# Performance work log

Measured on AMD Instinct MI355X. Metric: run time of the kernel, lower is better.

## Reference

```python
import jax, jax.numpy as jnp
import numpy as np

B, N, H, EH = 4, 512, 128, 128


def _init_linear(key, fan_in, fan_out, scale=0.02):
    W = jax.random.normal(key, (fan_in, fan_out), dtype=jnp.float32) * scale
    b = jnp.zeros((fan_out,), dtype=jnp.float32)
    return W, b


def setup_inputs() -> dict:
    key = jax.random.key(0)
    ks = jax.random.split(key, 9)
    h = jax.random.normal(ks[0], (B, N, H), dtype=jnp.float32)
    x = jax.random.normal(ks[1], (B, N, 3), dtype=jnp.float32)
    We1, be1 = _init_linear(ks[2], 2 * H + 1, EH)
    We2, be2 = _init_linear(ks[3], EH, H)
    Wc1, bc1 = _init_linear(ks[4], H, EH)
    Wc2, bc2 = _init_linear(ks[5], EH, 1)
    Wc2 = Wc2 * 0.1  # coord_mlp[-1].weight.mul_(0.1)
    Wn1, bn1 = _init_linear(ks[6], 2 * H, EH)
    Wn2, bn2 = _init_linear(ks[7], EH, H)
    return {
        "h": h, "x": x,
        "We1": We1, "be1": be1, "We2": We2, "be2": be2,
        "Wc1": Wc1, "bc1": bc1, "Wc2": Wc2, "bc2": bc2,
        "Wn1": Wn1, "bn1": bn1, "Wn2": Wn2, "bn2": bn2,
        "radius": 2,
    }


def reference(h, x, We1, be1, We2, be2, Wc1, bc1, Wc2, bc2, Wn1, bn1, Wn2, bn2, radius):
    silu = jax.nn.silu
    Hd = h.shape[-1]
    # pairwise geometry
    dx = x[:, :, None, :] - x[:, None, :, :]            # [B,N,N,3]
    d2 = jnp.sum(dx * dx, axis=-1, keepdims=True)       # [B,N,N,1]
    n = h.shape[1]
    eye = jnp.eye(n, dtype=bool)[None]                  # [1,N,N]
    mask = (d2[..., 0] < float(radius) ** 2) & ~eye     # [B,N,N]
    mask_f = mask[..., None].astype(h.dtype)            # [B,N,N,1]
    # edge MLP: split concat([h_i,h_j,d2]) @ We1 into three small matmuls
    pre = (jnp.einsum('bnh,he->bne', h, We1[:Hd])[:, :, None, :]
           + jnp.einsum('bnh,he->bne', h, We1[Hd:2 * Hd])[:, None, :, :]
           + d2 * We1[2 * Hd] + be1)                    # [B,N,N,EH]
    m_ij = silu(silu(pre) @ We2 + be2) * mask_f          # [B,N,N,H]
    agg = m_ij.sum(axis=2)                               # [B,N,H]
    # coord update
    gate = silu(m_ij @ Wc1 + bc1) @ Wc2 + bc2            # [B,N,N,1]
    coord_delta = jnp.sum(dx * gate * mask_f, axis=2)    # [B,N,3]
    n_neighbors = jnp.clip(mask.sum(axis=-1, keepdims=True), 1, None).astype(dx.dtype)
    x_new = x + coord_delta / n_neighbors
    # node update
    h_cat = jnp.concatenate([h, agg], axis=-1)           # [B,N,2H]
    h_new = h + (silu(h_cat @ Wn1 + bn1) @ Wn2 + bn2)
    return h_new, x_new
```

## Files before the change

kernel.cpp:

```cpp
#include <hip/hip_runtime.h>

#define BB 4
#define NN 512
#define HH 128
#define EHH 128
#define JB 64

typedef short short8 __attribute__((ext_vector_type(8)));
typedef float f32x4 __attribute__((ext_vector_type(4)));

__device__ __forceinline__ float fsilu(float x){
    float e = __expf(-x);
    return x * __builtin_amdgcn_rcpf(1.0f + e);
}

__device__ __forceinline__ unsigned int cvt_pk_bf16(float lo, float hi){
    unsigned int r;
    asm("v_cvt_pk_bf16_f32 %0, %1, %2" : "=v"(r) : "v"(lo), "v"(hi));
    return r;
}

__device__ __forceinline__ unsigned short f2bf(float f){
    return (unsigned short)(cvt_pk_bf16(f, 0.f) & 0xffffu);
}

__device__ __forceinline__ unsigned int cvt_pk_fp8(float lo, float hi){
    unsigned int r;
    asm("v_cvt_pk_fp8_f32 %0, %1, %2" : "=v"(r) : "v"(lo), "v"(hi));
    return r;
}

__global__ __launch_bounds__(256) void k_prep(
    const float* __restrict__ h,
    const float* __restrict__ We1, const float* __restrict__ be1,
    const float* __restrict__ We2, const float* __restrict__ Wc1,
    float* __restrict__ hi_e, unsigned short* __restrict__ hj_eb,
    unsigned short* __restrict__ We2T, unsigned char* __restrict__ Wc1F8)
{
    const int tid = threadIdx.x;
    if (blockIdx.x < BB*NN/8) {
        __shared__ float hrows[8][HH];
        const int row0 = blockIdx.x * 8;
        #pragma unroll
        for (int t = tid; t < 8*HH; t += 256)
            hrows[t >> 7][t & 127] = h[row0*HH + t];
        __syncthreads();
        const int col  = tid & 127;
        const int half = tid >> 7;
        float acc[8] = {0.f,0.f,0.f,0.f,0.f,0.f,0.f,0.f};
        #pragma unroll 4
        for (int k = 0; k < HH; ++k){
            float w = We1[(half*HH + k)*EHH + col];
            #pragma unroll
            for (int r = 0; r < 8; ++r) acc[r] += hrows[r][k] * w;
        }
        if (half == 0){
            const float bb = be1[col];
            #pragma unroll
            for (int r = 0; r < 8; ++r)
                hi_e[(row0 + r)*EHH + col] = acc[r] + bb;
        } else {
            #pragma unroll
            for (int r = 0; r < 8; ++r)
                hj_eb[(row0 + r)*EHH + col] = f2bf(acc[r]);
        }
    } else {
        const int bid = blockIdx.x - BB*NN/8;
        for (int t = bid*256 + tid; t < 128*128; t += 16*256){
            int o = t >> 7, kk = t & 127;
            We2T[t] = f2bf(We2[kk*HH + o]);
        }
        for (int idx = bid*256 + tid; idx < 8192; idx += 16*256){
            int o = idx >> 6, kp = idx & 63;
            int k = 2*kp;
            unsigned int pk = cvt_pk_fp8(Wc1[k*EHH + o] * 16.f,
                                         Wc1[(k+1)*EHH + o] * 16.f);
            *(unsigned short*)&Wc1F8[o*EHH + k] = (unsigned short)(pk & 0xffffu);
        }
    }
}

__global__ __launch_bounds__(256, 2) void k_edge(
    const float* __restrict__ x,
    const float* __restrict__ hi_e,
    const unsigned short* __restrict__ hj_eb,
    const unsigned short* __restrict__ We2T,
    const unsigned char* __restrict__ Wc1F8,
    const float* __restrict__ We1,
    const float* __restrict__ be2,
    const float* __restrict__ bc1,
    const float* __restrict__ wc2,
    const float* __restrict__ bc2p,
    const int* __restrict__ radius,
    float* __restrict__ aggb, float* __restrict__ xout)
{
    __shared__ unsigned short A1[JB][136];
    __shared__ unsigned char  mA8[JB][136];
    __shared__ float dxs[2][JB][4];
    __shared__ float his[HH], w3s[HH];
    __shared__ float aggp[2][HH];
    __shared__ float cred[4][3];
    __shared__ unsigned short jseg[4][128];
    __shared__ unsigned short jlist[NN];
    __shared__ int cnts[4];

    const int tid  = threadIdx.x;
    const int lane = tid & 63;
    const int wave = tid >> 6;
    const int l15  = lane & 15;
    const int g    = lane >> 4;
    const int wm   = wave >> 1, wn = wave & 1;

    const int b = blockIdx.x >> 9;
    const int i = blockIdx.x & (NN-1);
    const int base = b*NN;

    if (tid < HH){
        his[tid] = hi_e[(base + i)*EHH + tid];
        w3s[tid] = We1[2*HH*EHH + tid];
    }
    const float xi0 = x[(base+i)*3+0];
    const float xi1 = x[(base+i)*3+1];
    const float xi2 = x[(base+i)*3+2];
    const int   rad = radius[0];
    const float r2  = (float)(rad*rad);
    const float bc2v = bc2p[0];

    float be2r[4], bc1r[4], wc2r[4];
    #pragma unroll
    for (int nt = 0; nt < 4; ++nt){
        const int col = wn*64 + nt*16 + l15;
        be2r[nt] = be2[col];
        bc1r[nt] = bc1[col];
        wc2r[nt] = wc2[col];
    }

    short8 bW1[4][4];
    long   bW2[4][4];
    #pragma unroll
    for (int nt = 0; nt < 4; ++nt){
        const int col = wn*64 + nt*16 + l15;
        #pragma unroll
        for (int ks = 0; ks < 4; ++ks){
            bW1[nt][ks] = *(const short8*)&We2T[col*EHH + ks*32 + g*8];
            bW2[nt][ks] = *(const long*)&Wc1F8[col*EHH + ks*32 + g*8];
        }
    }

    int wcnt = 0;
    #pragma unroll
    for (int t = 0; t < 2; ++t){
        const int j = wave*128 + t*64 + lane;
        float xj0 = x[(base+j)*3+0];
        float xj1 = x[(base+j)*3+1];
        float xj2 = x[(base+j)*3+2];
        float d0 = xi0-xj0, d1 = xi1-xj1, d2c = xi2-xj2;
        float d2v = d0*d0 + d1*d1 + d2c*d2c;
        bool pass = (d2v < r2) && (j != i);
        unsigned long long bal = __ballot(pass);
        int pos = __popcll(bal & ((1ull << lane) - 1ull));
        if (pass) jseg[wave][wcnt + pos] = (unsigned short)j;
        wcnt += __popcll(bal);
    }
    if (lane == 0) cnts[wave] = wcnt;
    __syncthreads();
    const int c0n = cnts[0], c1n = cnts[1], c2n = cnts[2], c3n = cnts[3];
    const int total = c0n + c1n + c2n + c3n;
    const int off = (wave > 0 ? c0n : 0) + (wave > 1 ? c1n : 0) + (wave > 2 ? c2n : 0);
    for (int k2 = lane; k2 < wcnt; k2 += 64)
        jlist[off + k2] = jseg[wave][k2];
    __syncthreads();

    const int nch = (total + JB - 1) / JB;

    float agg[4] = {0.f, 0.f, 0.f, 0.f};
    float cx = 0.f, cy = 0.f, cz = 0.f;

    short8 hjn[4];
    float xjn0 = 0.f, xjn1 = 0.f, xjn2 = 0.f, mfn = 0.f;
    if (nch > 0){
        const int idx = lane;
        const int vld = idx < total;
        const int jn = vld ? jlist[idx] : jlist[total-1];
        mfn = vld ? 1.f : 0.f;
        #pragma unroll
        for (int k = 0; k < 4; ++k)
            hjn[k] = *(const short8*)&hj_eb[(base + jn)*EHH + wave*32 + k*8];
        xjn0 = x[(base+jn)*3+0];
        xjn1 = x[(base+jn)*3+1];
        xjn2 = x[(base+jn)*3+2];
    }

    #pragma unroll 1
    for (int c = 0; c < nch; ++c){
        const int buf = c & 1;
        const int r = lane;

        float d0 = xi0 - xjn0;
        float d1 = xi1 - xjn1;
        float d2c = xi2 - xjn2;
        float d2v = d0*d0 + d1*d1 + d2c*d2c;
        float mf = mfn;
        if (wave == 0){
            dxs[buf][r][0] = d0; dxs[buf][r][1] = d1;
            dxs[buf][r][2] = d2c; dxs[buf][r][3] = mf;
            float t = mf * bc2v;
            cx += d0*t; cy += d1*t; cz += d2c*t;
        }
        const int sw = ((r>>3)&1)<<3;
        #pragma unroll
        for (int k = 0; k < 4; ++k){
            const int c0 = wave*32 + k*8;
            short8 hj8 = hjn[k];
            f32x4 hiA = *(const f32x4*)&his[c0];
            f32x4 hiB = *(const f32x4*)&his[c0+4];
            f32x4 w3A = *(const f32x4*)&w3s[c0];
            f32x4 w3B = *(const f32x4*)&w3s[c0+4];
            float p[8];
            #pragma unroll
            for (int e = 0; e < 4; ++e){
                float hv0 = __uint_as_float(((unsigned int)(unsigned short)hj8[e]) << 16);
                float hv1 = __uint_as_float(((unsigned int)(unsigned short)hj8[e+4]) << 16);
                p[e]   = fsilu(hiA[e] + hv0 + d2v*w3A[e]);
                p[e+4] = fsilu(hiB[e] + hv1 + d2v*w3B[e]);
            }
            short8 outv;
            ((unsigned int*)&outv)[0] = cvt_pk_bf16(p[0], p[1]);
            ((unsigned int*)&outv)[1] = cvt_pk_bf16(p[2], p[3]);
            ((unsigned int*)&outv)[2] = cvt_pk_bf16(p[4], p[5]);
            ((unsigned int*)&outv)[3] = cvt_pk_bf16(p[6], p[7]);
            *(short8*)&A1[r][c0 ^ sw] = outv;
        }
        if (c + 1 < nch){
            const int idx = (c+1)*JB + lane;
            const int vld = idx < total;
            const int jn = vld ? jlist[idx] : jlist[total-1];
            mfn = vld ? 1.f : 0.f;
            #pragma unroll
            for (int k = 0; k < 4; ++k)
                hjn[k] = *(const short8*)&hj_eb[(base + jn)*EHH + wave*32 + k*8];
            xjn0 = x[(base+jn)*3+0];
            xjn1 = x[(base+jn)*3+1];
            xjn2 = x[(base+jn)*3+2];
        }
        __syncthreads();

        f32x4 acc[2][4];
        #pragma unroll
        for (int mt = 0; mt < 2; ++mt)
            #pragma unroll
            for (int nt = 0; nt < 4; ++nt) acc[mt][nt] = (f32x4){0.f,0.f,0.f,0.f};

        const int swr = ((l15>>3)&1)<<3;
        #pragma unroll
        for (int ks = 0; ks < 4; ++ks){
            short8 afr[2];
            #pragma unroll
            for (int mt = 0; mt < 2; ++mt){
                const int row = wm*32 + mt*16 + l15;
                afr[mt] = *(const short8*)&A1[row][(ks*32 + g*8) ^ swr];
            }
            #pragma unroll
            for (int nt = 0; nt < 4; ++nt)
                #pragma unroll
                for (int mt = 0; mt < 2; ++mt)
                    acc[mt][nt] = __builtin_amdgcn_mfma_f32_16x16x32_bf16(
                        afr[mt], bW1[nt][ks], acc[mt][nt], 0, 0, 0);
        }

        #pragma unroll
        for (int mt = 0; mt < 2; ++mt){
            float mfr[4];
            #pragma unroll
            for (int rg = 0; rg < 4; ++rg)
                mfr[rg] = dxs[buf][wm*32 + mt*16 + g*4 + rg][3];
            #pragma unroll
            for (int nt = 0; nt < 4; ++nt){
                const int col = wn*64 + nt*16 + l15;
                f32x4 v = acc[mt][nt];
                #pragma unroll
                for (int rg = 0; rg < 4; ++rg){
                    const int row = wm*32 + mt*16 + g*4 + rg;
                    float m = fsilu(v[rg] + be2r[nt]) * mfr[rg];
                    agg[nt] += m;
                    mA8[row][col] = (unsigned char)(cvt_pk_fp8(m * 8.f, 0.f) & 0xffu);
                }
            }
        }
        __syncthreads();

        f32x4 acc2[2][4];
        #pragma unroll
        for (int mt = 0; mt < 2; ++mt)
            #pragma unroll
            for (int nt = 0; nt < 4; ++nt) acc2[mt][nt] = (f32x4){0.f,0.f,0.f,0.f};

        #pragma unroll
        for (int ks = 0; ks < 4; ++ks){
            long a8[2];
            #pragma unroll
            for (int mt = 0; mt < 2; ++mt){
                const int row = wm*32 + mt*16 + l15;
                a8[mt] = *(const long*)&mA8[row][ks*32 + g*8];
            }
            #pragma unroll
            for (int nt = 0; nt < 4; ++nt)
                #pragma unroll
                for (int mt = 0; mt < 2; ++mt)
                    acc2[mt][nt] = __builtin_amdgcn_mfma_f32_16x16x32_fp8_fp8(
                        a8[mt], bW2[nt][ks], acc2[mt][nt], 0, 0, 0);
        }

        float gp[2][4];
        #pragma unroll
        for (int mt = 0; mt < 2; ++mt)
            #pragma unroll
            for (int rg = 0; rg < 4; ++rg) gp[mt][rg] = 0.f;
        #pragma unroll
        for (int mt = 0; mt < 2; ++mt)
            #pragma unroll
            for (int nt = 0; nt < 4; ++nt){
                f32x4 v = acc2[mt][nt];
                #pragma unroll
                for (int rg = 0; rg < 4; ++rg)
                    gp[mt][rg] += fsilu(v[rg]*(1.f/128.f) + bc1r[nt]) * wc2r[nt];
            }
        #pragma unroll
        for (int mt = 0; mt < 2; ++mt)
            #pragma unroll
            for (int rg = 0; rg < 4; ++rg){
                const int row = wm*32 + mt*16 + g*4 + rg;
                f32x4 dv = *(const f32x4*)&dxs[buf][row][0];
                float gv = gp[mt][rg] * dv[3];
                cx += dv[0]*gv; cy += dv[1]*gv; cz += dv[2]*gv;
            }
    }

    #pragma unroll
    for (int nt = 0; nt < 4; ++nt){
        float t = agg[nt];
        t += __shfl_xor(t, 16); t += __shfl_xor(t, 32);
        agg[nt] = t;
    }
    if (lane < 16){
        #pragma unroll
        for (int nt = 0; nt < 4; ++nt)
            aggp[wm][wn*64 + nt*16 + l15] = agg[nt];
    }

    #pragma unroll
    for (int m = 1; m <= 32; m <<= 1){
        cx += __shfl_xor(cx, m);
        cy += __shfl_xor(cy, m);
        cz += __shfl_xor(cz, m);
    }
    if (lane == 0){
        cred[wave][0] = cx; cred[wave][1] = cy; cred[wave][2] = cz;
    }
    __syncthreads();
    if (tid < HH) aggb[(base + i)*HH + tid] = aggp[0][tid] + aggp[1][tid];
    if (tid == 0){
        float sx = cred[0][0] + cred[1][0] + cred[2][0] + cred[3][0];
        float sy = cred[0][1] + cred[1][1] + cred[2][1] + cred[3][1];
        float sz = cred[0][2] + cred[1][2] + cred[2][2] + cred[3][2];
        float inv = 1.0f / (float)(total > 0 ? total : 1);
        xout[(base+i)*3 + 0] = xi0 + sx*inv;
        xout[(base+i)*3 + 1] = xi1 + sy*inv;
        xout[(base+i)*3 + 2] = xi2 + sz*inv;
    }
}

__global__ __launch_bounds__(128) void k_node(
    const float* __restrict__ h, const float* __restrict__ aggb,
    const float* __restrict__ Wn1, const float* __restrict__ bn1,
    const float* __restrict__ Wn2, const float* __restrict__ bn2,
    float* __restrict__ hout)
{
    __shared__ float hcat[8][260];
    __shared__ float t1[8][132];
    const int tid = threadIdx.x;
    const int row0 = blockIdx.x * 8;
    #pragma unroll
    for (int r = 0; r < 8; ++r){
        hcat[r][tid]      = h[(row0 + r)*HH + tid];
        hcat[r][HH + tid] = aggb[(row0 + r)*HH + tid];
    }
    __syncthreads();
    float acc[8] = {0.f,0.f,0.f,0.f,0.f,0.f,0.f,0.f};
    #pragma unroll 4
    for (int k = 0; k < 2*HH; ++k){
        float w = Wn1[k*EHH + tid];
        #pragma unroll
        for (int r = 0; r < 8; ++r) acc[r] += hcat[r][k] * w;
    }
    const float bn1v = bn1[tid];
    #pragma unroll
    for (int r = 0; r < 8; ++r) t1[r][tid] = fsilu(acc[r] + bn1v);
    __syncthreads();
    float acc2[8] = {0.f,0.f,0.f,0.f,0.f,0.f,0.f,0.f};
    #pragma unroll 4
    for (int e = 0; e < EHH; ++e){
        float w = Wn2[e*HH + tid];
        #pragma unroll
        for (int r = 0; r < 8; ++r) acc2[r] += t1[r][e] * w;
    }
    const float bn2v = bn2[tid];
    #pragma unroll
    for (int r = 0; r < 8; ++r)
        hout[(row0 + r)*HH + tid] = hcat[r][tid] + acc2[r] + bn2v;
}

extern "C" void kernel_launch(void* const* d_in, const int* in_sizes, int n_in,
                              void* d_out, int out_size, void* d_ws, size_t ws_size,
                              hipStream_t stream) {
    const float* h   = (const float*)d_in[0];
    const float* x   = (const float*)d_in[1];
    const float* We1 = (const float*)d_in[2];
    const float* be1 = (const float*)d_in[3];
    const float* We2 = (const float*)d_in[4];
    const float* be2 = (const float*)d_in[5];
    const float* Wc1 = (const float*)d_in[6];
    const float* bc1 = (const float*)d_in[7];
    const float* Wc2 = (const float*)d_in[8];
    const float* bc2 = (const float*)d_in[9];
    const float* Wn1 = (const float*)d_in[10];
    const float* bn1 = (const float*)d_in[11];
    const float* Wn2 = (const float*)d_in[12];
    const float* bn2 = (const float*)d_in[13];
    const int* radius = (const int*)d_in[14];

    float* out_h = (float*)d_out;
    float* out_x = out_h + BB*NN*HH;

    char* ws = (char*)d_ws;
    float*          hi_e  = (float*)ws;
    unsigned short* hj_eb = (unsigned short*)(ws + (1u<<20));
    unsigned short* We2T  = (unsigned short*)(ws + (1u<<20) + (512u<<10));
    unsigned char*  Wc1F8 = (unsigned char*)(ws + (1u<<20) + (544u<<10));
    float*          aggb  = (float*)(ws + (1u<<20) + (560u<<10));

    k_prep<<<BB*NN/8 + 16, 256, 0, stream>>>(h, We1, be1, We2, Wc1,
                                             hi_e, hj_eb, We2T, Wc1F8);
    k_edge<<<BB*NN, 256, 0, stream>>>(x, hi_e, hj_eb, We2T, Wc1F8,
                                      We1, be2, bc1, Wc2, bc2, radius,
                                      aggb, out_x);
    k_node<<<BB*NN/8, 128, 0, stream>>>(h, aggb, Wn1, bn1, Wn2, bn2, out_h);
}
```

Before: 236.8 us.

## Process one node per wave with 16-neighbor chunks and shared LDS weights

The edge kernel now gives each wave its own node i, so one 256-thread block handles four nodes. Each wave walks its own neighbor list in chunks of 16 and computes all 128 output columns itself. The bf16 and fp8 weight matrices are staged once per block into shared memory instead of being held in per-wave registers. Intermediate A fragments stay in registers and the per-chunk block barriers disappear, so waves no longer synchronise with each other. The cost is many more LDS reads of the B weights per MFMA, smaller MFMA tiles per chunk, and per-wave load imbalance when neighbor counts differ.

```diff
diff --git a/kernel.cpp b/kernel.cpp
--- a/kernel.cpp
+++ b/kernel.cpp
@@ -4,10 +4,11 @@
 #define NN 512
 #define HH 128
 #define EHH 128
-#define JB 64
+#define JC 16
 
 typedef short short8 __attribute__((ext_vector_type(8)));
 typedef float f32x4 __attribute__((ext_vector_type(4)));
+typedef int   int4v __attribute__((ext_vector_type(4)));
 
 __device__ __forceinline__ float fsilu(float x){
     float e = __expf(-x);
@@ -94,30 +95,45 @@
     const int* __restrict__ radius,
     float* __restrict__ aggb, float* __restrict__ xout)
 {
-    __shared__ unsigned short A1[JB][136];
-    __shared__ unsigned char  mA8[JB][136];
-    __shared__ float dxs[2][JB][4];
-    __shared__ float his[HH], w3s[HH];
-    __shared__ float aggp[2][HH];
-    __shared__ float cred[4][3];
-    __shared__ unsigned short jseg[4][128];
-    __shared__ unsigned short jlist[NN];
-    __shared__ int cnts[4];
+    __shared__ unsigned short We2T_s[128][136];
+    __shared__ unsigned char  Wc1F8_s[128][144];
+    __shared__ unsigned short jlist[4][NN];
+    __shared__ unsigned char  mA8[4][JC][136];
 
     const int tid  = threadIdx.x;
     const int lane = tid & 63;
     const int wave = tid >> 6;
     const int l15  = lane & 15;
     const int g    = lane >> 4;
-    const int wm   = wave >> 1, wn = wave & 1;
-
-    const int b = blockIdx.x >> 9;
-    const int i = blockIdx.x & (NN-1);
-    const int base = b*NN;
-
-    if (tid < HH){
-        his[tid] = hi_e[(base + i)*EHH + tid];
-        w3s[tid] = We1[2*HH*EHH + tid];
+
+    const int b    = blockIdx.x >> 7;
+    const int i    = (blockIdx.x & 127) * 4 + wave;
+    const int base = b * NN;
+
+    for (int t = tid; t < 128*16; t += 256){
+        int row = t >> 4, seg = t & 15;
+        *(short8*)&We2T_s[row][seg*8] = *(const short8*)&We2T[row*EHH + seg*8];
+    }
+    for (int t = tid; t < 128*8; t += 256){
+        int row = t >> 3, seg = t & 7;
+        *(int4v*)&Wc1F8_s[row][seg*16] = *(const int4v*)&Wc1F8[row*EHH + seg*16];
+    }
+
+    f32x4 hiA[4], hiB[4], w3A[4], w3B[4];
+    #pragma unroll
+    for (int ks = 0; ks < 4; ++ks){
+        hiA[ks] = *(const f32x4*)&hi_e[(base+i)*EHH + ks*32 + g*8];
+        hiB[ks] = *(const f32x4*)&hi_e[(base+i)*EHH + ks*32 + g*8 + 4];
+        w3A[ks] = *(const f32x4*)&We1[2*HH*EHH + ks*32 + g*8];
+        w3B[ks] = *(const f32x4*)&We1[2*HH*EHH + ks*32 + g*8 + 4];
+    }
+    float be2r[8], bc1r[8], wc2r[8];
+    #pragma unroll
+    for (int nt = 0; nt < 8; ++nt){
+        const int col = nt*16 + l15;
+        be2r[nt] = be2[col];
+        bc1r[nt] = bc1[col];
+        wc2r[nt] = wc2[col];
     }
     const float xi0 = x[(base+i)*3+0];
     const float xi1 = x[(base+i)*3+1];
@@ -126,31 +142,10 @@
     const float r2  = (float)(rad*rad);
     const float bc2v = bc2p[0];
 
-    float be2r[4], bc1r[4], wc2r[4];
-    #pragma unroll
-    for (int nt = 0; nt < 4; ++nt){
-        const int col = wn*64 + nt*16 + l15;
-        be2r[nt] = be2[col];
-        bc1r[nt] = bc1[col];
-        wc2r[nt] = wc2[col];
-    }
-
-    short8 bW1[4][4];
-    long   bW2[4][4];
-    #pragma unroll
-    for (int nt = 0; nt < 4; ++nt){
-        const int col = wn*64 + nt*16 + l15;
-        #pragma unroll
-        for (int ks = 0; ks < 4; ++ks){
-            bW1[nt][ks] = *(const short8*)&We2T[col*EHH + ks*32 + g*8];
-            bW2[nt][ks] = *(const long*)&Wc1F8[col*EHH + ks*32 + g*8];
-        }
-    }
-
-    int wcnt = 0;
-    #pragma unroll
-    for (int t = 0; t < 2; ++t){
-        const int j = wave*128 + t*64 + lane;
+    int cnt = 0;
+    #pragma unroll 1
+    for (int t = 0; t < NN/64; ++t){
+        const int j = t*64 + lane;
         float xj0 = x[(base+j)*3+0];
         float xj1 = x[(base+j)*3+1];
         float xj2 = x[(base+j)*3+2];
@@ -159,214 +154,157 @@
         bool pass = (d2v < r2) && (j != i);
         unsigned long long bal = __ballot(pass);
         int pos = __popcll(bal & ((1ull << lane) - 1ull));
-        if (pass) jseg[wave][wcnt + pos] = (unsigned short)j;
-        wcnt += __popcll(bal);
-    }
-    if (lane == 0) cnts[wave] = wcnt;
+        if (pass) jlist[wave][cnt + pos] = (unsigned short)j;
+        cnt += __popcll(bal);
+    }
+
     __syncthreads();
-    const int c0n = cnts[0], c1n = cnts[1], c2n = cnts[2], c3n = cnts[3];
-    const int total = c0n + c1n + c2n + c3n;
-    const int off = (wave > 0 ? c0n : 0) + (wave > 1 ? c1n : 0) + (wave > 2 ? c2n : 0);
-    for (int k2 = lane; k2 < wcnt; k2 += 64)
-        jlist[off + k2] = jseg[wave][k2];
-    __syncthreads();
-
-    const int nch = (total + JB - 1) / JB;
-
-    float agg[4] = {0.f, 0.f, 0.f, 0.f};
+
+    const int nch = (cnt + JC - 1) / JC;
+
+    float agg[8] = {0.f,0.f,0.f,0.f,0.f,0.f,0.f,0.f};
     float cx = 0.f, cy = 0.f, cz = 0.f;
 
-    short8 hjn[4];
-    float xjn0 = 0.f, xjn1 = 0.f, xjn2 = 0.f, mfn = 0.f;
+    short8 hjp[4];
+    float xjp0 = 0.f, xjp1 = 0.f, xjp2 = 0.f;
     if (nch > 0){
-        const int idx = lane;
-        const int vld = idx < total;
-        const int jn = vld ? jlist[idx] : jlist[total-1];
-        mfn = vld ? 1.f : 0.f;
-        #pragma unroll
-        for (int k = 0; k < 4; ++k)
-            hjn[k] = *(const short8*)&hj_eb[(base + jn)*EHH + wave*32 + k*8];
-        xjn0 = x[(base+jn)*3+0];
-        xjn1 = x[(base+jn)*3+1];
-        xjn2 = x[(base+jn)*3+2];
+        int idx = l15 < cnt ? l15 : cnt-1;
+        int jn = jlist[wave][idx];
+        #pragma unroll
+        for (int ks = 0; ks < 4; ++ks)
+            hjp[ks] = *(const short8*)&hj_eb[(base+jn)*EHH + ks*32 + g*8];
+        xjp0 = x[(base+jn)*3+0];
+        xjp1 = x[(base+jn)*3+1];
+        xjp2 = x[(base+jn)*3+2];
     }
 
     #pragma unroll 1
     for (int c = 0; c < nch; ++c){
-        const int buf = c & 1;
-        const int r = lane;
-
-        float d0 = xi0 - xjn0;
-        float d1 = xi1 - xjn1;
-        float d2c = xi2 - xjn2;
+        float d0 = xi0 - xjp0;
+        float d1 = xi1 - xjp1;
+        float d2c = xi2 - xjp2;
         float d2v = d0*d0 + d1*d1 + d2c*d2c;
-        float mf = mfn;
-        if (wave == 0){
-            dxs[buf][r][0] = d0; dxs[buf][r][1] = d1;
-            dxs[buf][r][2] = d2c; dxs[buf][r][3] = mf;
-            float t = mf * bc2v;
-            cx += d0*t; cy += d1*t; cz += d2c*t;
-        }
-        const int sw = ((r>>3)&1)<<3;
-        #pragma unroll
-        for (int k = 0; k < 4; ++k){
-            const int c0 = wave*32 + k*8;
-            short8 hj8 = hjn[k];
-            f32x4 hiA = *(const f32x4*)&his[c0];
-            f32x4 hiB = *(const f32x4*)&his[c0+4];
-            f32x4 w3A = *(const f32x4*)&w3s[c0];
-            f32x4 w3B = *(const f32x4*)&w3s[c0+4];
+        short8 a1[4];
+        #pragma unroll
+        for (int ks = 0; ks < 4; ++ks){
+            short8 hj8 = hjp[ks];
             float p[8];
             #pragma unroll
             for (int e = 0; e < 4; ++e){
                 float hv0 = __uint_as_float(((unsigned int)(unsigned short)hj8[e]) << 16);
                 float hv1 = __uint_as_float(((unsigned int)(unsigned short)hj8[e+4]) << 16);
-                p[e]   = fsilu(hiA[e] + hv0 + d2v*w3A[e]);
-                p[e+4] = fsilu(hiB[e] + hv1 + d2v*w3B[e]);
+                p[e]   = fsilu(hiA[ks][e] + hv0 + d2v*w3A[ks][e]);
+                p[e+4] = fsilu(hiB[ks][e] + hv1 + d2v*w3B[ks][e]);
             }
             short8 outv;
             ((unsigned int*)&outv)[0] = cvt_pk_bf16(p[0], p[1]);
             ((unsigned int*)&outv)[1] = cvt_pk_bf16(p[2], p[3]);
             ((unsigned int*)&outv)[2] = cvt_pk_bf16(p[4], p[5]);
             ((unsigned int*)&outv)[3] = cvt_pk_bf16(p[6], p[7]);
-            *(short8*)&A1[r][c0 ^ sw] = outv;
+            a1[ks] = outv;
         }
         if (c + 1 < nch){
-            const int idx = (c+1)*JB + lane;
-            const int vld = idx < total;
-            const int jn = vld ? jlist[idx] : jlist[total-1];
-            mfn = vld ? 1.f : 0.f;
-            #pragma unroll
-            for (int k = 0; k < 4; ++k)
-                hjn[k] = *(const short8*)&hj_eb[(base + jn)*EHH + wave*32 + k*8];
-            xjn0 = x[(base+jn)*3+0];
-            xjn1 = x[(base+jn)*3+1];
-            xjn2 = x[(base+jn)*3+2];
-        }
-        __syncthreads();
-
-        f32x4 acc[2][4];
-        #pragma unroll
-        for (int mt = 0; mt < 2; ++mt)
-            #pragma unroll
-            for (int nt = 0; nt < 4; ++nt) acc[mt][nt] = (f32x4){0.f,0.f,0.f,0.f};
-
-        const int swr = ((l15>>3)&1)<<3;
+            int idx = (c+1)*JC + l15;
+            idx = idx < cnt ? idx : cnt-1;
+            int jn = jlist[wave][idx];
+            #pragma unroll
+            for (int ks = 0; ks < 4; ++ks)
+                hjp[ks] = *(const short8*)&hj_eb[(base+jn)*EHH + ks*32 + g*8];
+            xjp0 = x[(base+jn)*3+0];
+            xjp1 = x[(base+jn)*3+1];
+            xjp2 = x[(base+jn)*3+2];
+        }
+
+        f32x4 acc1[8];
+        #pragma unroll
+        for (int nt = 0; nt < 8; ++nt) acc1[nt] = (f32x4){0.f,0.f,0.f,0.f};
         #pragma unroll
         for (int ks = 0; ks < 4; ++ks){
-            short8 afr[2];
-            #pragma unroll
-            for (int mt = 0; mt < 2; ++mt){
-                const int row = wm*32 + mt*16 + l15;
-                afr[mt] = *(const short8*)&A1[row][(ks*32 + g*8) ^ swr];
-            }
-            #pragma unroll
-            for (int nt = 0; nt < 4; ++nt)
-                #pragma unroll
-                for (int mt = 0; mt < 2; ++mt)
-                    acc[mt][nt] = __builtin_amdgcn_mfma_f32_16x16x32_bf16(
-                        afr[mt], bW1[nt][ks], acc[mt][nt], 0, 0, 0);
-        }
-
-        #pragma unroll
-        for (int mt = 0; mt < 2; ++mt){
-            float mfr[4];
+            #pragma unroll
+            for (int nt = 0; nt < 8; ++nt){
+                short8 bf = *(const short8*)&We2T_s[nt*16 + l15][ks*32 + g*8];
+                acc1[nt] = __builtin_amdgcn_mfma_f32_16x16x32_bf16(
+                    a1[ks], bf, acc1[nt], 0, 0, 0);
+            }
+        }
+
+        float mfr[4];
+        #pragma unroll
+        for (int rg = 0; rg < 4; ++rg)
+            mfr[rg] = (c*JC + 4*g + rg < cnt) ? 1.f : 0.f;
+        #pragma unroll
+        for (int nt = 0; nt < 8; ++nt){
+            f32x4 v = acc1[nt];
+            #pragma unroll
+            for (int rg = 0; rg < 4; ++rg){
+                float m = fsilu(v[rg] + be2r[nt]) * mfr[rg];
+                agg[nt] += m;
+                mA8[wave][4*g + rg][nt*16 + l15] =
+                    (unsigned char)(cvt_pk_fp8(m * 8.f, 0.f) & 0xffu);
+            }
+        }
+
+        long a8[4];
+        #pragma unroll
+        for (int ks = 0; ks < 4; ++ks)
+            a8[ks] = *(const long*)&mA8[wave][l15][ks*32 + g*8];
+        f32x4 acc2[8];
+        #pragma unroll
+        for (int nt = 0; nt < 8; ++nt) acc2[nt] = (f32x4){0.f,0.f,0.f,0.f};
+        #pragma unroll
+        for (int ks = 0; ks < 4; ++ks){
+            #pragma unroll
+            for (int nt = 0; nt < 8; ++nt){
+                long bf8 = *(const long*)&Wc1F8_s[nt*16 + l15][ks*32 + g*8];
+                acc2[nt] = __builtin_amdgcn_mfma_f32_16x16x32_fp8_fp8(
+                    a8[ks], bf8, acc2[nt], 0, 0, 0);
+            }
+        }
+
+        float gp[4] = {0.f, 0.f, 0.f, 0.f};
+        #pragma unroll
+        for (int nt = 0; nt < 8; ++nt){
+            f32x4 v = acc2[nt];
             #pragma unroll
             for (int rg = 0; rg < 4; ++rg)
-                mfr[rg] = dxs[buf][wm*32 + mt*16 + g*4 + rg][3];
-            #pragma unroll
-            for (int nt = 0; nt < 4; ++nt){
-                const int col = wn*64 + nt*16 + l15;
-                f32x4 v = acc[mt][nt];
-                #pragma unroll
-                for (int rg = 0; rg < 4; ++rg){
-                    const int row = wm*32 + mt*16 + g*4 + rg;
-                    float m = fsilu(v[rg] + be2r[nt]) * mfr[rg];
-                    agg[nt] += m;
-                    mA8[row][col] = (unsigned char)(cvt_pk_fp8(m * 8.f, 0.f) & 0xffu);
-                }
-            }
-        }
-        __syncthreads();
-
-        f32x4 acc2[2][4];
-        #pragma unroll
-        for (int mt = 0; mt < 2; ++mt)
-            #pragma unroll
-            for (int nt = 0; nt < 4; ++nt) acc2[mt][nt] = (f32x4){0.f,0.f,0.f,0.f};
-
-        #pragma unroll
-        for (int ks = 0; ks < 4; ++ks){
-            long a8[2];
-            #pragma unroll
-            for (int mt = 0; mt < 2; ++mt){
-                const int row = wm*32 + mt*16 + l15;
-                a8[mt] = *(const long*)&mA8[row][ks*32 + g*8];
-            }
-            #pragma unroll
-            for (int nt = 0; nt < 4; ++nt)
-                #pragma unroll
-                for (int mt = 0; mt < 2; ++mt)
-                    acc2[mt][nt] = __builtin_amdgcn_mfma_f32_16x16x32_fp8_fp8(
-                        a8[mt], bW2[nt][ks], acc2[mt][nt], 0, 0, 0);
-        }
-
-        float gp[2][4];
-        #pragma unroll
-        for (int mt = 0; mt < 2; ++mt)
-            #pragma unroll
-            for (int rg = 0; rg < 4; ++rg) gp[mt][rg] = 0.f;
-        #pragma unroll
-        for (int mt = 0; mt < 2; ++mt)
-            #pragma unroll
-            for (int nt = 0; nt < 4; ++nt){
-                f32x4 v = acc2[mt][nt];
-                #pragma unroll
-                for (int rg = 0; rg < 4; ++rg)
-                    gp[mt][rg] += fsilu(v[rg]*(1.f/128.f) + bc1r[nt]) * wc2r[nt];
-            }
-        #pragma unroll
-        for (int mt = 0; mt < 2; ++mt)
-            #pragma unroll
-            for (int rg = 0; rg < 4; ++rg){
-                const int row = wm*32 + mt*16 + g*4 + rg;
-                f32x4 dv = *(const f32x4*)&dxs[buf][row][0];
-                float gv = gp[mt][rg] * dv[3];
-                cx += dv[0]*gv; cy += dv[1]*gv; cz += dv[2]*gv;
-            }
-    }
-
-    #pragma unroll
-    for (int nt = 0; nt < 4; ++nt){
+                gp[rg] += fsilu(v[rg]*(1.f/128.f) + bc1r[nt]) * wc2r[nt];
+        }
+        #pragma unroll
+        for (int rg = 0; rg < 4; ++rg){
+            float t = gp[rg];
+            t += __shfl_xor(t, 1); t += __shfl_xor(t, 2);
+            t += __shfl_xor(t, 4); t += __shfl_xor(t, 8);
+            float gv = (t + bc2v) * mfr[rg];
+            const int row = 4*g + rg;
+            float dx0 = __shfl(d0, row);
+            float dx1 = __shfl(d1, row);
+            float dx2 = __shfl(d2c, row);
+            if (l15 == 0){
+                cx += dx0*gv; cy += dx1*gv; cz += dx2*gv;
+            }
+        }
+    }
+
+    #pragma unroll
+    for (int nt = 0; nt < 8; ++nt){
         float t = agg[nt];
         t += __shfl_xor(t, 16); t += __shfl_xor(t, 32);
         agg[nt] = t;
     }
     if (lane < 16){
         #pragma unroll
-        for (int nt = 0; nt < 4; ++nt)
-            aggp[wm][wn*64 + nt*16 + l15] = agg[nt];
-    }
-
-    #pragma unroll
-    for (int m = 1; m <= 32; m <<= 1){
-        cx += __shfl_xor(cx, m);
-        cy += __shfl_xor(cy, m);
-        cz += __shfl_xor(cz, m);
-    }
+        for (int nt = 0; nt < 8; ++nt)
+            aggb[(base + i)*HH + nt*16 + lane] = agg[nt];
+    }
+
+    cx += __shfl_xor(cx, 16); cx += __shfl_xor(cx, 32);
+    cy += __shfl_xor(cy, 16); cy += __shfl_xor(cy, 32);
+    cz += __shfl_xor(cz, 16); cz += __shfl_xor(cz, 32);
     if (lane == 0){
-        cred[wave][0] = cx; cred[wave][1] = cy; cred[wave][2] = cz;
-    }
-    __syncthreads();
-    if (tid < HH) aggb[(base + i)*HH + tid] = aggp[0][tid] + aggp[1][tid];
-    if (tid == 0){
-        float sx = cred[0][0] + cred[1][0] + cred[2][0] + cred[3][0];
-        float sy = cred[0][1] + cred[1][1] + cred[2][1] + cred[3][1];
-        float sz = cred[0][2] + cred[1][2] + cred[2][2] + cred[3][2];
-        float inv = 1.0f / (float)(total > 0 ? total : 1);
-        xout[(base+i)*3 + 0] = xi0 + sx*inv;
-        xout[(base+i)*3 + 1] = xi1 + sy*inv;
-        xout[(base+i)*3 + 2] = xi2 + sz*inv;
+        float inv = 1.0f / (float)(cnt > 0 ? cnt : 1);
+        xout[(base+i)*3 + 0] = xi0 + cx*inv;
+        xout[(base+i)*3 + 1] = xi1 + cy*inv;
+        xout[(base+i)*3 + 2] = xi2 + cz*inv;
     }
 }
 
@@ -441,8 +379,8 @@
 
     k_prep<<<BB*NN/8 + 16, 256, 0, stream>>>(h, We1, be1, We2, Wc1,
                                              hi_e, hj_eb, We2T, Wc1F8);
-    k_edge<<<BB*NN, 256, 0, stream>>>(x, hi_e, hj_eb, We2T, Wc1F8,
-                                      We1, be2, bc1, Wc2, bc2, radius,
-                                      aggb, out_x);
+    k_edge<<<BB*NN/4, 256, 0, stream>>>(x, hi_e, hj_eb, We2T, Wc1F8,
+                                        We1, be2, bc1, Wc2, bc2, radius,
+                                        aggb, out_x);
     k_node<<<BB*NN/8, 128, 0, stream>>>(h, aggb, Wn1, bn1, Wn2, bn2, out_h);
 }
```

Measured after the change: 249.8 us. 5.5% more time.
